# Performance work log

Measured on AMD Instinct MI355X. Metric: run time of the kernel, lower is better.

Reference implementation:

```python
import jax, jax.numpy as jnp
import numpy as np


def setup_inputs() -> dict:
    key = jax.random.key(0)
    k1, k2, k3, k4, k5 = jax.random.split(key, 5)
    B, C, D = 16384, 1000, 2048
    x = jax.random.normal(k1, (B, D), dtype=jnp.float32)
    W = jax.random.normal(k2, (C, D), dtype=jnp.float32) * 0.02  # fc weight
    b = jax.random.normal(k3, (C,), dtype=jnp.float32) * 0.01
    selector_weights = jax.random.normal(k4, (5,), dtype=jnp.float32) * 0.01
    selector_thresholds = jax.random.normal(k5, (5,), dtype=jnp.float32) * 0.01
    ensemble_threshold = jnp.zeros((1,), dtype=jnp.float32)
    return {
        "x": x, "W": W, "b": b,
        "selector_weights": selector_weights,
        "selector_thresholds": selector_thresholds,
        "ensemble_threshold": ensemble_threshold,
    }


def _selector_scores(logits, W):
    # top-2 of raw logits (RLConfM): sorted descending -> top_k(2)
    top2, _ = jax.lax.top_k(logits, 2)
    conf_m = top2[:, 0] - top2[:, 1]
    # geometric margin (RLGeoM): logits normalized by row norms of fc weight
    w_norms = jnp.linalg.norm(W, axis=1)                      # [C]
    norm_logits = logits / (w_norms + 1e-8)[None, :]          # [B, C]
    ntop2, _ = jax.lax.top_k(norm_logits, 2)
    geo_m = ntop2[:, 0] - ntop2[:, 1]
    # softmax-based selectors share one softmax pass
    probs = jax.nn.softmax(logits, axis=1)                    # [B, C]
    sr_max = jnp.max(probs, axis=1)
    doctor = 1.0 - 1.0 / jnp.sum(probs * probs, axis=1)
    neg_entropy = jnp.sum(probs * jnp.log(probs + 1e-10), axis=1)  # = -entropy
    # order matches nn.ModuleList: [SRMax, SRDoctor, SREntropy, RLGeoM, RLConfM]
    return jnp.stack([sr_max, doctor, neg_entropy, geo_m, conf_m], axis=1)  # [B, 5]


def reference(x, W, b, selector_weights, selector_thresholds, ensemble_threshold):
    # base model runs under no_grad in the original
    logits = jax.lax.stop_gradient(jnp.dot(x, W.T) + b)       # [B, C]
    scores = _selector_scores(logits, jax.lax.stop_gradient(W))  # [B, 5]
    indicators = jnp.tanh(scores - selector_thresholds[None, :])  # [B, 5]
    ensemble = jnp.sum(selector_weights[None, :] * indicators, axis=1)  # [B]
    selection_score = jnp.tanh(ensemble - ensemble_threshold[0])
    return (logits, selection_score)
```

## Files before the change

### kernel.cpp

```cpp
#include <hip/hip_runtime.h>
#include <stdint.h>

#define B_ROWS 16384
#define C_COLS 1000
#define D_DIM  2048

typedef __bf16 bf16x8 __attribute__((ext_vector_type(8)));
typedef float  f32x4  __attribute__((ext_vector_type(4)));
typedef unsigned short u16;

__device__ __forceinline__ u16 f2bf(float f) {
  union { float f; uint32_t u; } v; v.f = f;
  return (u16)((v.u + 0x7FFFu + ((v.u >> 16) & 1u)) >> 16);
}

__global__ __launch_bounds__(256)
void prep(const float* __restrict__ W, const float* __restrict__ x,
          u16* __restrict__ Wb, u16* __restrict__ xb, float* __restrict__ norms) {
  const int r = blockIdx.x;
  const int t = threadIdx.x;
  const bool isW = (r < C_COLS);
  const float* src = isW ? (W + (size_t)r * D_DIM)
                         : (x + (size_t)(r - C_COLS) * D_DIM);
  u16* dst = isW ? (Wb + (size_t)r * D_DIM)
                 : (xb + (size_t)(r - C_COLS) * D_DIM);
  const int c = t * 8;
  float4 v0 = *reinterpret_cast<const float4*>(src + c);
  float4 v1 = *reinterpret_cast<const float4*>(src + c + 4);
  uint32_t p0 = (uint32_t)f2bf(v0.x) | ((uint32_t)f2bf(v0.y) << 16);
  uint32_t p1 = (uint32_t)f2bf(v0.z) | ((uint32_t)f2bf(v0.w) << 16);
  uint32_t p2 = (uint32_t)f2bf(v1.x) | ((uint32_t)f2bf(v1.y) << 16);
  uint32_t p3 = (uint32_t)f2bf(v1.z) | ((uint32_t)f2bf(v1.w) << 16);
  const int row_id = isW ? r : (r - C_COLS);
  const int m2 = (row_id & 7) << 3;
  uint4 val; val.x = p0; val.y = p1; val.z = p2; val.w = p3;
  *reinterpret_cast<uint4*>(dst + (c ^ m2)) = val;
  if (isW) {
    float ss = v0.x*v0.x + v0.y*v0.y + v0.z*v0.z + v0.w*v0.w
             + v1.x*v1.x + v1.y*v1.y + v1.z*v1.z + v1.w*v1.w;
    #pragma unroll
    for (int m = 32; m; m >>= 1) ss += __shfl_xor(ss, m);
    __shared__ float wss[4];
    if ((t & 63) == 0) wss[t >> 6] = ss;
    __syncthreads();
    if (t == 0) norms[r] = sqrtf(wss[0] + wss[1] + wss[2] + wss[3]);
  }
}

#define ABASE(B,H) (((B)*2+(H))*8192)
#define BBASE(B,H) (32768 + ((B)*2+(H))*8192)

#define STAGE_A(BUF,H,OFF) { _Pragma("unroll") for (int j_=0;j_<2;++j_){ \
    u16* d_ = lds + ABASE(BUF,H) + (j_*64 + w*8)*64; \
    __builtin_amdgcn_global_load_lds( \
      (const __attribute__((address_space(1))) void*)(sa[H][j_] + (OFF)), \
      (__attribute__((address_space(3))) void*)d_, 16, 0, 0); } }

#define STAGE_B(BUF,H,OFF) { _Pragma("unroll") for (int j_=0;j_<2;++j_){ \
    u16* d_ = lds + BBASE(BUF,H) + (j_*64 + w*8)*64; \
    __builtin_amdgcn_global_load_lds( \
      (const __attribute__((address_space(1))) void*)(sb[H][j_] + (OFF)), \
      (__attribute__((address_space(3))) void*)d_, 16, 0, 0); } }

#define READ_A(BUF,MH) { _Pragma("unroll") for (int ks_=0;ks_<2;++ks_) \
  _Pragma("unroll") for (int fr_=0;fr_<4;++fr_) \
    Acur[ks_][fr_] = *reinterpret_cast<const bf16x8*>( \
        pA[ks_] + ((BUF)*2+(MH))*16384 + fr_*2048); }

#define READ_B(BUF,NH,DST) { _Pragma("unroll") for (int ks_=0;ks_<2;++ks_) \
  _Pragma("unroll") for (int fc_=0;fc_<2;++fc_) \
    DST[ks_][fc_] = *reinterpret_cast<const bf16x8*>( \
        pB[ks_] + ((BUF)*2+(NH))*16384 + fc_*2048); }

#define MMA(MH,NH,BSRC) { \
  __builtin_amdgcn_s_setprio(1); \
  _Pragma("unroll") for (int ks_=0;ks_<2;++ks_) \
    _Pragma("unroll") for (int fr_=0;fr_<4;++fr_) \
      _Pragma("unroll") for (int fc_=0;fc_<2;++fc_) \
        acc[MH][fr_][NH][fc_] = __builtin_amdgcn_mfma_f32_16x16x32_bf16( \
            Acur[ks_][fr_], BSRC[ks_][fc_], acc[MH][fr_][NH][fc_], 0, 0, 0); \
  __builtin_amdgcn_s_setprio(0); }

#define BAR  __builtin_amdgcn_s_barrier()
#define LG0  asm volatile("s_waitcnt lgkmcnt(0)" ::: "memory")
#define LG8  asm volatile("s_waitcnt lgkmcnt(8)" ::: "memory")
#define SCHB __builtin_amdgcn_sched_barrier(0)
#define VM4  asm volatile("s_waitcnt vmcnt(4)" ::: "memory")
#define VM0  asm volatile("s_waitcnt vmcnt(0)" ::: "memory")

#define SMERGE(m_,s_,q_,u_,om_,os_,oq_,ou_) { \
    float M_ = fmaxf(m_, om_); \
    float a_ = __expf(m_ - M_), b_ = __expf(om_ - M_); \
    float ns_ = a_*s_ + b_*os_; \
    float nq_ = a_*a_*q_ + b_*b_*oq_; \
    float nu_ = a_*(u_ + (m_-M_)*s_) + b_*(ou_ + (om_-M_)*os_); \
    m_ = M_; s_ = ns_; q_ = nq_; u_ = nu_; }

#define T2MERGE(t1_,t2_,o1_,o2_) { \
    if (o1_ > t1_) { t2_ = fmaxf(t1_, o2_); t1_ = o1_; } else t2_ = fmaxf(t2_, o1_); }

template<int FUSE>
__global__ __launch_bounds__(512, 2)
void gemm8(const u16* __restrict__ xb, const u16* __restrict__ Wb,
           const float* __restrict__ bias, float* __restrict__ out,
           const float* __restrict__ norms, float* __restrict__ partials) {
  __shared__ u16 lds[65536];

  const int bid = blockIdx.x;
  const int swz = (bid & 7) * 32 + (bid >> 3);
  const int tm = swz >> 2, tn = swz & 3;
  const int m0 = tm * 256, n0 = tn * 256;

  const int t = threadIdx.x, w = t >> 6, l = t & 63;
  const int wr = w >> 2, wcn = w & 3;

  f32x4 acc[2][4][2][2];
  #pragma unroll
  for (int a = 0; a < 2; ++a)
    #pragma unroll
    for (int b2 = 0; b2 < 4; ++b2)
      #pragma unroll
      for (int c2 = 0; c2 < 2; ++c2)
        #pragma unroll
        for (int d2 = 0; d2 < 2; ++d2)
          acc[a][b2][c2][d2] = (f32x4){0.f, 0.f, 0.f, 0.f};

  bf16x8 Acur[2][4], B0c[2][2], B1c[2][2];

  const char* ldsc = (const char*)lds;
  const int la  = l & 15;
  const int hi3 = (l >> 4) << 3;
  const int m3  = (l & 7) << 3;
  const char* pA[2];
  const char* pB[2];
  pA[0] = ldsc + wr*8192 + la*128 + (((0  + hi3) ^ m3) << 1);
  pA[1] = ldsc + wr*8192 + la*128 + (((32 + hi3) ^ m3) << 1);
  pB[0] = ldsc + 65536 + (wcn*32 + la)*128 + (((0  + hi3) ^ m3) << 1);
  pB[1] = ldsc + 65536 + (wcn*32 + la)*128 + (((32 + hi3) ^ m3) << 1);

  const char* sa[2][2];
  const char* sb[2][2];
  #pragma unroll
  for (int H = 0; H < 2; ++H)
    #pragma unroll
    for (int j = 0; j < 2; ++j) {
      sa[H][j] = (const char*)xb +
        (((size_t)(m0 + H*128 + j*64 + w*8 + (l>>3))) * D_DIM + (l&7)*8) * 2;
      int gr = n0 + H*128 + j*64 + w*8 + (l>>3);
      if (gr >= C_COLS) gr = C_COLS - 1;
      sb[H][j] = (const char*)Wb + ((size_t)gr * D_DIM + (l&7)*8) * 2;
    }

  STAGE_A(0,0,0); STAGE_B(0,0,0); STAGE_A(0,1,0); STAGE_B(0,1,0);
  STAGE_A(1,0,128); STAGE_B(1,0,128);
  VM4;
  BAR;

  for (int it = 0; it < 15; ++it) {
    READ_A(0,0); READ_B(0,0,B0c); READ_B(0,1,B1c);
    STAGE_A(1,1,128); STAGE_B(1,1,128); LG8;
    BAR; LG0; SCHB; MMA(0,0,B0c); MMA(0,1,B1c); BAR;
    READ_A(0,1); STAGE_A(0,0,256); STAGE_B(0,0,256);
    BAR; LG0; SCHB; MMA(1,1,B1c); MMA(1,0,B0c); VM4; BAR;
    READ_A(1,0); READ_B(1,0,B0c); READ_B(1,1,B1c);
    STAGE_A(0,1,256); STAGE_B(0,1,256); LG8;
    BAR; LG0; SCHB; MMA(0,0,B0c); MMA(0,1,B1c); BAR;
    READ_A(1,1); STAGE_A(1,0,384); STAGE_B(1,0,384);
    BAR; LG0; SCHB; MMA(1,1,B1c); MMA(1,0,B0c); VM4; BAR;
    #pragma unroll
    for (int H = 0; H < 2; ++H)
      #pragma unroll
      for (int j = 0; j < 2; ++j) { sa[H][j] += 256; sb[H][j] += 256; }
  }
  READ_A(0,0); READ_B(0,0,B0c); READ_B(0,1,B1c);
  STAGE_A(1,1,128); STAGE_B(1,1,128); LG8;
  BAR; LG0; SCHB; MMA(0,0,B0c); MMA(0,1,B1c); BAR;
  READ_A(0,1);
  BAR; LG0; SCHB; MMA(1,1,B1c); MMA(1,0,B0c); VM0; BAR;
  READ_A(1,0); READ_B(1,0,B0c); READ_B(1,1,B1c); LG8;
  BAR; LG0; SCHB; MMA(0,0,B0c); MMA(0,1,B1c); BAR;
  READ_A(1,1);
  BAR; LG0; SCHB; MMA(1,1,B1c); MMA(1,0,B0c);

  float bv[2][2]; bool okc[2][2];
  #pragma unroll
  for (int nh = 0; nh < 2; ++nh)
    #pragma unroll
    for (int fc = 0; fc < 2; ++fc) {
      int col = n0 + nh*128 + wcn*32 + fc*16 + (l & 15);
      okc[nh][fc] = (col < C_COLS);
      bv[nh][fc]  = okc[nh][fc] ? bias[col] : 0.f;
    }

  #pragma unroll
  for (int mh = 0; mh < 2; ++mh)
    #pragma unroll
    for (int nh = 0; nh < 2; ++nh)
      #pragma unroll
      for (int fc = 0; fc < 2; ++fc)
        if (okc[nh][fc]) {
          int col = n0 + nh*128 + wcn*32 + fc*16 + (l & 15);
          #pragma unroll
          for (int fr = 0; fr < 4; ++fr) {
            int row0 = m0 + mh*128 + wr*64 + fr*16 + ((l >> 4) << 2);
            #pragma unroll
            for (int j = 0; j < 4; ++j)
              out[(size_t)(row0 + j) * C_COLS + col] = acc[mh][fr][nh][fc][j] + bv[nh][fc];
          }
        }

  if constexpr (FUSE) {
    float* sf = (float*)lds;
    const int rrow = t >> 2;
    const int q    = t & 3;
    BAR;
    #pragma unroll
    for (int mh = 0; mh < 2; ++mh) {
      #pragma unroll
      for (int fr = 0; fr < 4; ++fr)
        #pragma unroll
        for (int j = 0; j < 4; ++j) {
          int rl = wr*64 + fr*16 + ((l >> 4) << 2) + j;
          int sw = (rl & 7) << 2;
          #pragma unroll
          for (int nh = 0; nh < 2; ++nh)
            #pragma unroll
            for (int fc = 0; fc < 2; ++fc) {
              int c = nh*128 + wcn*32 + fc*16 + (l & 15);
              sf[rl*256 + (c ^ sw)] = acc[mh][fr][nh][fc][j] + bv[nh][fc];
            }
        }
      LG0; BAR;
      float m=-3.4e38f, t1=-3.4e38f, t2=-3.4e38f, n1=-3.4e38f, n2=-3.4e38f;
      #pragma unroll
      for (int i = 0; i < 16; ++i) {
        int U = q*16 + i;
        f32x4 v4 = *reinterpret_cast<const f32x4*>(
            &sf[rrow*256 + 4*(U ^ (rrow & 7))]);
        f32x4 w4 = *reinterpret_cast<const f32x4*>(&norms[n0 + 4*U]);
        #pragma unroll
        for (int e = 0; e < 4; ++e) {
          int col = n0 + 4*U + e;
          if (col < C_COLS) {
            float v = v4[e];
            m = fmaxf(m, v);
            if (v > t1) { t2 = t1; t1 = v; } else if (v > t2) t2 = v;
            float nv = v / (w4[e] + 1e-8f);
            if (nv > n1) { n2 = n1; n1 = nv; } else if (nv > n2) n2 = nv;
          }
        }
      }
      float s = 0.f, qq = 0.f, u = 0.f;
      #pragma unroll
      for (int i = 0; i < 16; ++i) {
        int U = q*16 + i;
        f32x4 v4 = *reinterpret_cast<const f32x4*>(
            &sf[rrow*256 + 4*(U ^ (rrow & 7))]);
        #pragma unroll
        for (int e = 0; e < 4; ++e) {
          int col = n0 + 4*U + e;
          if (col < C_COLS) {
            float d = v4[e] - m;
            float ee = __expf(d);
            s += ee; qq += ee*ee; u += d*ee;
          }
        }
      }
      LG0;
      #pragma unroll
      for (int msk = 1; msk < 4; msk <<= 1) {
        float o1 = __shfl_xor(t1, msk), o2 = __shfl_xor(t2, msk);
        T2MERGE(t1, t2, o1, o2);
        float p1 = __shfl_xor(n1, msk), p2 = __shfl_xor(n2, msk);
        T2MERGE(n1, n2, p1, p2);
        float om = __shfl_xor(m, msk), os = __shfl_xor(s, msk);
        float oq = __shfl_xor(qq, msk), ou = __shfl_xor(u, msk);
        SMERGE(m, s, qq, u, om, os, oq, ou);
      }
      if (q == 0) {
        float* pp = partials + ((size_t)(m0 + mh*128 + rrow) * 4 + tn) * 8;
        float4 lo; lo.x=t1; lo.y=t2; lo.z=n1; lo.w=n2;
        float4 hi; hi.x=m;  hi.y=s;  hi.z=qq; hi.w=u;
        *reinterpret_cast<float4*>(pp)     = lo;
        *reinterpret_cast<float4*>(pp + 4) = hi;
      }
      if (mh == 0) { BAR; }
    }
  }
}

__global__ __launch_bounds__(256)
void selector2(const float* __restrict__ partials,
               const float* __restrict__ selw, const float* __restrict__ selt,
               const float* __restrict__ ethr, float* __restrict__ out2) {
  const int row = blockIdx.x * 256 + threadIdx.x;
  const float* pp = partials + (size_t)row * 32;
  float P[4][8];
  #pragma unroll
  for (int wv = 0; wv < 4; ++wv) {
    float4 lo = *reinterpret_cast<const float4*>(pp + wv*8);
    float4 hi = *reinterpret_cast<const float4*>(pp + wv*8 + 4);
    P[wv][0]=lo.x; P[wv][1]=lo.y; P[wv][2]=lo.z; P[wv][3]=lo.w;
    P[wv][4]=hi.x; P[wv][5]=hi.y; P[wv][6]=hi.z; P[wv][7]=hi.w;
  }
  float t1=P[0][0], t2=P[0][1], n1=P[0][2], n2=P[0][3];
  float m=P[0][4], s=P[0][5], q=P[0][6], u=P[0][7];
  #pragma unroll
  for (int wv = 1; wv < 4; ++wv) {
    T2MERGE(t1, t2, P[wv][0], P[wv][1]);
    T2MERGE(n1, n2, P[wv][2], P[wv][3]);
    SMERGE(m, s, q, u, P[wv][4], P[wv][5], P[wv][6], P[wv][7]);
  }
  float sc0 = 1.f / s;
  float sc1 = 1.f - (s * s) / q;
  float sc2 = u / s - __logf(s);
  float sc3 = n1 - n2;
  float sc4 = t1 - t2;
  float ens = selw[0] * tanhf(sc0 - selt[0])
            + selw[1] * tanhf(sc1 - selt[1])
            + selw[2] * tanhf(sc2 - selt[2])
            + selw[3] * tanhf(sc3 - selt[3])
            + selw[4] * tanhf(sc4 - selt[4]);
  out2[row] = tanhf(ens - ethr[0]);
}

__global__ __launch_bounds__(256)
void selector(const float* __restrict__ logits, const float* __restrict__ norms,
              const float* __restrict__ selw, const float* __restrict__ selt,
              const float* __restrict__ ethr, float* __restrict__ out) {
  __shared__ float nrm[1024];
  const int t = threadIdx.x;
  #pragma unroll
  for (int i = 0; i < 4; ++i) {
    int idx = t + i * 256;
    nrm[idx] = (idx < C_COLS) ? norms[idx] : 1.0f;
  }
  __syncthreads();
  const int w = t >> 6, l = t & 63;
  const int row = blockIdx.x * 4 + w;
  const float* lp = logits + (size_t)row * C_COLS;
  float lg[16];
  float t1 = -3.4e38f, t2 = -3.4e38f, n1 = -3.4e38f, n2 = -3.4e38f;
  #pragma unroll
  for (int i = 0; i < 4; ++i) {
    float4 v4 = *reinterpret_cast<const float4*>(lp + l * 4 + i * 256);
    #pragma unroll
    for (int j = 0; j < 4; ++j) {
      int idx = l * 4 + i * 256 + j;
      float raw = (j == 0) ? v4.x : (j == 1) ? v4.y : (j == 2) ? v4.z : v4.w;
      bool ok = (idx < C_COLS);
      float v = ok ? raw : -3.4e38f;
      lg[i * 4 + j] = v;
      if (v > t1) { t2 = t1; t1 = v; } else if (v > t2) t2 = v;
      float nv = ok ? raw / (nrm[idx] + 1e-8f) : -3.4e38f;
      if (nv > n1) { n2 = n1; n1 = nv; } else if (nv > n2) n2 = nv;
    }
  }
  #pragma unroll
  for (int m = 1; m < 64; m <<= 1) {
    float o1 = __shfl_xor(t1, m), o2 = __shfl_xor(t2, m);
    T2MERGE(t1, t2, o1, o2);
    float p1 = __shfl_xor(n1, m), p2 = __shfl_xor(n2, m);
    T2MERGE(n1, n2, p1, p2);
  }
  const float mx = t1;
  float S = 0.f, sq = 0.f;
  float ex[16];
  #pragma unroll
  for (int i = 0; i < 16; ++i) {
    float e = (lg[i] > -1e38f) ? __expf(lg[i] - mx) : 0.f;
    ex[i] = e; S += e; sq += e * e;
  }
  #pragma unroll
  for (int m = 1; m < 64; m <<= 1) { S += __shfl_xor(S, m); sq += __shfl_xor(sq, m); }
  float ent = 0.f;
  #pragma unroll
  for (int i = 0; i < 16; ++i)
    if (lg[i] > -1e38f) { float p = ex[i] / S; ent += p * __logf(p + 1e-10f); }
  #pragma unroll
  for (int m = 1; m < 64; m <<= 1) ent += __shfl_xor(ent, m);
  if (l == 0) {
    float ens = selw[0] * tanhf(1.f / S - selt[0])
              + selw[1] * tanhf(1.f - (S * S) / sq - selt[1])
              + selw[2] * tanhf(ent - selt[2])
              + selw[3] * tanhf(n1 - n2 - selt[3])
              + selw[4] * tanhf(t1 - t2 - selt[4]);
    out[row] = tanhf(ens - ethr[0]);
  }
}

extern "C" void kernel_launch(void* const* d_in, const int* in_sizes, int n_in,
                              void* d_out, int out_size, void* d_ws, size_t ws_size,
                              hipStream_t stream) {
  const float* x    = (const float*)d_in[0];
  const float* W    = (const float*)d_in[1];
  const float* b    = (const float*)d_in[2];
  const float* selw = (const float*)d_in[3];
  const float* selt = (const float*)d_in[4];
  const float* ethr = (const float*)d_in[5];
  float* out = (float*)d_out;
  float* out2 = out + (size_t)B_ROWS * C_COLS;

  u16*   Wb    = (u16*)d_ws;
  float* norms = (float*)((char*)d_ws + 4096000);
  u16*   xb    = (u16*)((char*)d_ws + 4100096);
  float* parts = (float*)((char*)d_ws + 4100096 + 67108864);

  const size_t need_fuse = 4100096 + 67108864 + 2097152;
  const size_t need_r4   = 4100096 + 67108864;

  if (ws_size >= need_fuse) {
    prep<<<C_COLS + B_ROWS, 256, 0, stream>>>(W, x, Wb, xb, norms);
    gemm8<1><<<256, 512, 0, stream>>>(xb, Wb, b, out, norms, parts);
    selector2<<<B_ROWS / 256, 256, 0, stream>>>(parts, selw, selt, ethr, out2);
  } else if (ws_size >= need_r4) {
    prep<<<C_COLS + B_ROWS, 256, 0, stream>>>(W, x, Wb, xb, norms);
    gemm8<0><<<256, 512, 0, stream>>>(xb, Wb, b, out, norms, nullptr);
    selector<<<B_ROWS / 4, 256, 0, stream>>>(out, norms, selw, selt, ethr, out2);
  }
}
```

Measured before the change: 124.0 us.

## Split MFMA by k-step with partial LDS waits and coalesce fused logits stores

The main loop now issues LDS fragment reads per k-substep. It waits only for the first substep's reads (lgkmcnt 8 or 4) before starting its MFMAs, so the second substep's LDS reads overlap with matrix math, and priority is raised across the whole MMA block. In the fused epilogue, logits are no longer scattered straight from MFMA accumulators to global memory. They are written as float4 vectors from the swizzled LDS tile already built for the selector reduction. The column interleave is changed so the four threads of a row write adjacent chunks. This adds a dependency on the finer waitcnt accounting and on C being a multiple of 4.

```diff
diff --git a/kernel.cpp b/kernel.cpp
--- a/kernel.cpp
+++ b/kernel.cpp
@@ -62,31 +62,30 @@
       (const __attribute__((address_space(1))) void*)(sb[H][j_] + (OFF)), \
       (__attribute__((address_space(3))) void*)d_, 16, 0, 0); } }
 
-#define READ_A(BUF,MH) { _Pragma("unroll") for (int ks_=0;ks_<2;++ks_) \
+#define READ_A_KS(BUF,MH,KS) { _Pragma("unroll") for (int fr_=0;fr_<4;++fr_) \
+    Acur[KS][fr_] = *reinterpret_cast<const bf16x8*>( \
+        pA[KS] + ((BUF)*2+(MH))*16384 + fr_*2048); }
+
+#define READ_B_KS(BUF,NH,DST,KS) { _Pragma("unroll") for (int fc_=0;fc_<2;++fc_) \
+    DST[KS][fc_] = *reinterpret_cast<const bf16x8*>( \
+        pB[KS] + ((BUF)*2+(NH))*16384 + fc_*2048); }
+
+#define MMAK(MH,NH,BSRC,KS) { \
   _Pragma("unroll") for (int fr_=0;fr_<4;++fr_) \
-    Acur[ks_][fr_] = *reinterpret_cast<const bf16x8*>( \
-        pA[ks_] + ((BUF)*2+(MH))*16384 + fr_*2048); }
-
-#define READ_B(BUF,NH,DST) { _Pragma("unroll") for (int ks_=0;ks_<2;++ks_) \
-  _Pragma("unroll") for (int fc_=0;fc_<2;++fc_) \
-    DST[ks_][fc_] = *reinterpret_cast<const bf16x8*>( \
-        pB[ks_] + ((BUF)*2+(NH))*16384 + fc_*2048); }
-
-#define MMA(MH,NH,BSRC) { \
-  __builtin_amdgcn_s_setprio(1); \
-  _Pragma("unroll") for (int ks_=0;ks_<2;++ks_) \
-    _Pragma("unroll") for (int fr_=0;fr_<4;++fr_) \
-      _Pragma("unroll") for (int fc_=0;fc_<2;++fc_) \
-        acc[MH][fr_][NH][fc_] = __builtin_amdgcn_mfma_f32_16x16x32_bf16( \
-            Acur[ks_][fr_], BSRC[ks_][fc_], acc[MH][fr_][NH][fc_], 0, 0, 0); \
-  __builtin_amdgcn_s_setprio(0); }
-
-#define BAR  __builtin_amdgcn_s_barrier()
-#define LG0  asm volatile("s_waitcnt lgkmcnt(0)" ::: "memory")
-#define LG8  asm volatile("s_waitcnt lgkmcnt(8)" ::: "memory")
-#define SCHB __builtin_amdgcn_sched_barrier(0)
-#define VM4  asm volatile("s_waitcnt vmcnt(4)" ::: "memory")
-#define VM0  asm volatile("s_waitcnt vmcnt(0)" ::: "memory")
+    _Pragma("unroll") for (int fc_=0;fc_<2;++fc_) \
+      acc[MH][fr_][NH][fc_] = __builtin_amdgcn_mfma_f32_16x16x32_bf16( \
+          Acur[KS][fr_], BSRC[KS][fc_], acc[MH][fr_][NH][fc_], 0, 0, 0); }
+
+#define BAR   __builtin_amdgcn_s_barrier()
+#define LG0   asm volatile("s_waitcnt lgkmcnt(0)" ::: "memory")
+#define LGK0  asm volatile("s_waitcnt lgkmcnt(0)" ::: "memory")
+#define LGK4  asm volatile("s_waitcnt lgkmcnt(4)" ::: "memory")
+#define LGK8  asm volatile("s_waitcnt lgkmcnt(8)" ::: "memory")
+#define SCHB  __builtin_amdgcn_sched_barrier(0)
+#define VM4   asm volatile("s_waitcnt vmcnt(4)" ::: "memory")
+#define VM0   asm volatile("s_waitcnt vmcnt(0)" ::: "memory")
+#define SETP1 __builtin_amdgcn_s_setprio(1)
+#define SETP0 __builtin_amdgcn_s_setprio(0)
 
 #define SMERGE(m_,s_,q_,u_,om_,os_,oq_,ou_) { \
     float M_ = fmaxf(m_, om_); \
@@ -157,30 +156,67 @@
   BAR;
 
   for (int it = 0; it < 15; ++it) {
-    READ_A(0,0); READ_B(0,0,B0c); READ_B(0,1,B1c);
-    STAGE_A(1,1,128); STAGE_B(1,1,128); LG8;
-    BAR; LG0; SCHB; MMA(0,0,B0c); MMA(0,1,B1c); BAR;
-    READ_A(0,1); STAGE_A(0,0,256); STAGE_B(0,0,256);
-    BAR; LG0; SCHB; MMA(1,1,B1c); MMA(1,0,B0c); VM4; BAR;
-    READ_A(1,0); READ_B(1,0,B0c); READ_B(1,1,B1c);
-    STAGE_A(0,1,256); STAGE_B(0,1,256); LG8;
-    BAR; LG0; SCHB; MMA(0,0,B0c); MMA(0,1,B1c); BAR;
-    READ_A(1,1); STAGE_A(1,0,384); STAGE_B(1,0,384);
-    BAR; LG0; SCHB; MMA(1,1,B1c); MMA(1,0,B0c); VM4; BAR;
+    READ_A_KS(0,0,0); READ_B_KS(0,0,B0c,0); READ_B_KS(0,1,B1c,0);
+    READ_A_KS(0,0,1); READ_B_KS(0,0,B0c,1); READ_B_KS(0,1,B1c,1);
+    STAGE_A(1,1,128); STAGE_B(1,1,128);
+    BAR; LGK8; SETP1; SCHB;
+    MMAK(0,0,B0c,0); MMAK(0,1,B1c,0);
+    LGK0; SCHB;
+    MMAK(0,0,B0c,1); MMAK(0,1,B1c,1); SETP0;
+    BAR;
+    READ_A_KS(0,1,0); READ_A_KS(0,1,1);
+    STAGE_A(0,0,256); STAGE_B(0,0,256);
+    BAR; LGK4; SETP1; SCHB;
+    MMAK(1,1,B1c,0); MMAK(1,0,B0c,0);
+    LGK0; SCHB;
+    MMAK(1,1,B1c,1); MMAK(1,0,B0c,1); SETP0;
+    VM4; BAR;
+    READ_A_KS(1,0,0); READ_B_KS(1,0,B0c,0); READ_B_KS(1,1,B1c,0);
+    READ_A_KS(1,0,1); READ_B_KS(1,0,B0c,1); READ_B_KS(1,1,B1c,1);
+    STAGE_A(0,1,256); STAGE_B(0,1,256);
+    BAR; LGK8; SETP1; SCHB;
+    MMAK(0,0,B0c,0); MMAK(0,1,B1c,0);
+    LGK0; SCHB;
+    MMAK(0,0,B0c,1); MMAK(0,1,B1c,1); SETP0;
+    BAR;
+    READ_A_KS(1,1,0); READ_A_KS(1,1,1);
+    STAGE_A(1,0,384); STAGE_B(1,0,384);
+    BAR; LGK4; SETP1; SCHB;
+    MMAK(1,1,B1c,0); MMAK(1,0,B0c,0);
+    LGK0; SCHB;
+    MMAK(1,1,B1c,1); MMAK(1,0,B0c,1); SETP0;
+    VM4; BAR;
     #pragma unroll
     for (int H = 0; H < 2; ++H)
       #pragma unroll
       for (int j = 0; j < 2; ++j) { sa[H][j] += 256; sb[H][j] += 256; }
   }
-  READ_A(0,0); READ_B(0,0,B0c); READ_B(0,1,B1c);
-  STAGE_A(1,1,128); STAGE_B(1,1,128); LG8;
-  BAR; LG0; SCHB; MMA(0,0,B0c); MMA(0,1,B1c); BAR;
-  READ_A(0,1);
-  BAR; LG0; SCHB; MMA(1,1,B1c); MMA(1,0,B0c); VM0; BAR;
-  READ_A(1,0); READ_B(1,0,B0c); READ_B(1,1,B1c); LG8;
-  BAR; LG0; SCHB; MMA(0,0,B0c); MMA(0,1,B1c); BAR;
-  READ_A(1,1);
-  BAR; LG0; SCHB; MMA(1,1,B1c); MMA(1,0,B0c);
+  READ_A_KS(0,0,0); READ_B_KS(0,0,B0c,0); READ_B_KS(0,1,B1c,0);
+  READ_A_KS(0,0,1); READ_B_KS(0,0,B0c,1); READ_B_KS(0,1,B1c,1);
+  STAGE_A(1,1,128); STAGE_B(1,1,128);
+  BAR; LGK8; SETP1; SCHB;
+  MMAK(0,0,B0c,0); MMAK(0,1,B1c,0);
+  LGK0; SCHB;
+  MMAK(0,0,B0c,1); MMAK(0,1,B1c,1); SETP0;
+  BAR;
+  READ_A_KS(0,1,0); READ_A_KS(0,1,1);
+  BAR; LGK4; SETP1; SCHB;
+  MMAK(1,1,B1c,0); MMAK(1,0,B0c,0);
+  LGK0; SCHB;
+  MMAK(1,1,B1c,1); MMAK(1,0,B0c,1); SETP0;
+  VM0; BAR;
+  READ_A_KS(1,0,0); READ_B_KS(1,0,B0c,0); READ_B_KS(1,1,B1c,0);
+  READ_A_KS(1,0,1); READ_B_KS(1,0,B0c,1); READ_B_KS(1,1,B1c,1);
+  BAR; LGK8; SETP1; SCHB;
+  MMAK(0,0,B0c,0); MMAK(0,1,B1c,0);
+  LGK0; SCHB;
+  MMAK(0,0,B0c,1); MMAK(0,1,B1c,1); SETP0;
+  BAR;
+  READ_A_KS(1,1,0); READ_A_KS(1,1,1);
+  BAR; LGK4; SETP1; SCHB;
+  MMAK(1,1,B1c,0); MMAK(1,0,B0c,0);
+  LGK0; SCHB;
+  MMAK(1,1,B1c,1); MMAK(1,0,B0c,1); SETP0;
 
   float bv[2][2]; bool okc[2][2];
   #pragma unroll
@@ -192,22 +228,24 @@
       bv[nh][fc]  = okc[nh][fc] ? bias[col] : 0.f;
     }
 
-  #pragma unroll
-  for (int mh = 0; mh < 2; ++mh)
-    #pragma unroll
-    for (int nh = 0; nh < 2; ++nh)
-      #pragma unroll
-      for (int fc = 0; fc < 2; ++fc)
-        if (okc[nh][fc]) {
-          int col = n0 + nh*128 + wcn*32 + fc*16 + (l & 15);
-          #pragma unroll
-          for (int fr = 0; fr < 4; ++fr) {
-            int row0 = m0 + mh*128 + wr*64 + fr*16 + ((l >> 4) << 2);
+  if constexpr (!FUSE) {
+    #pragma unroll
+    for (int mh = 0; mh < 2; ++mh)
+      #pragma unroll
+      for (int nh = 0; nh < 2; ++nh)
+        #pragma unroll
+        for (int fc = 0; fc < 2; ++fc)
+          if (okc[nh][fc]) {
+            int col = n0 + nh*128 + wcn*32 + fc*16 + (l & 15);
             #pragma unroll
-            for (int j = 0; j < 4; ++j)
-              out[(size_t)(row0 + j) * C_COLS + col] = acc[mh][fr][nh][fc][j] + bv[nh][fc];
+            for (int fr = 0; fr < 4; ++fr) {
+              int row0 = m0 + mh*128 + wr*64 + fr*16 + ((l >> 4) << 2);
+              #pragma unroll
+              for (int j = 0; j < 4; ++j)
+                out[(size_t)(row0 + j) * C_COLS + col] = acc[mh][fr][nh][fc][j] + bv[nh][fc];
+            }
           }
-        }
+  }
 
   if constexpr (FUSE) {
     float* sf = (float*)lds;
@@ -234,10 +272,13 @@
       float m=-3.4e38f, t1=-3.4e38f, t2=-3.4e38f, n1=-3.4e38f, n2=-3.4e38f;
       #pragma unroll
       for (int i = 0; i < 16; ++i) {
-        int U = q*16 + i;
+        int U = i*4 + q;
         f32x4 v4 = *reinterpret_cast<const f32x4*>(
             &sf[rrow*256 + 4*(U ^ (rrow & 7))]);
         f32x4 w4 = *reinterpret_cast<const f32x4*>(&norms[n0 + 4*U]);
+        if (n0 + 4*U + 3 < C_COLS)
+          *reinterpret_cast<f32x4*>(
+              &out[(size_t)(m0 + mh*128 + rrow) * C_COLS + n0 + 4*U]) = v4;
         #pragma unroll
         for (int e = 0; e < 4; ++e) {
           int col = n0 + 4*U + e;
@@ -253,7 +294,7 @@
       float s = 0.f, qq = 0.f, u = 0.f;
       #pragma unroll
       for (int i = 0; i < 16; ++i) {
-        int U = q*16 + i;
+        int U = i*4 + q;
         f32x4 v4 = *reinterpret_cast<const f32x4*>(
             &sf[rrow*256 + 4*(U ^ (rrow & 7))]);
         #pragma unroll
```

Result: faster. 117.3 us (median of 4 runs) (-5.4%).

## Shrink GEMM tile to 128x128 with 1024 blocks and fused coalesced logit store

Applied to the files above, without the earlier changes.

The fused GEMM moves from 256x256 output tiles (256 blocks) to 128x128 tiles (1024 blocks). LDS drops to 64KB and launch bounds allow 4 blocks per CU. The pipeline becomes a simple two-buffer phase loop that waits for all loads (vmcnt 0) at each step, and the per-row selector partials grow from 4 to 8 column tiles. Fused logits are now written from LDS as coalesced float4 rows instead of strided per-lane stores. The aim is better occupancy and load balance across CUs and cheaper output stores, at the cost of less operand reuse per tile, more global traffic, and a less overlapped load schedule.

```diff
diff --git a/kernel.cpp b/kernel.cpp
--- a/kernel.cpp
+++ b/kernel.cpp
@@ -47,46 +47,51 @@
   }
 }
 
-#define ABASE(B,H) (((B)*2+(H))*8192)
-#define BBASE(B,H) (32768 + ((B)*2+(H))*8192)
-
-#define STAGE_A(BUF,H,OFF) { _Pragma("unroll") for (int j_=0;j_<2;++j_){ \
-    u16* d_ = lds + ABASE(BUF,H) + (j_*64 + w*8)*64; \
+#define STAGE_A(BUF,OFF) { _Pragma("unroll") for (int j_=0;j_<2;++j_){ \
+    u16* d_ = lds + (BUF)*8192 + (j_*64 + w*8)*64; \
     __builtin_amdgcn_global_load_lds( \
-      (const __attribute__((address_space(1))) void*)(sa[H][j_] + (OFF)), \
+      (const __attribute__((address_space(1))) void*)(sa[j_] + (OFF)), \
       (__attribute__((address_space(3))) void*)d_, 16, 0, 0); } }
 
-#define STAGE_B(BUF,H,OFF) { _Pragma("unroll") for (int j_=0;j_<2;++j_){ \
-    u16* d_ = lds + BBASE(BUF,H) + (j_*64 + w*8)*64; \
+#define STAGE_B(BUF,OFF) { _Pragma("unroll") for (int j_=0;j_<2;++j_){ \
+    u16* d_ = lds + 16384 + (BUF)*8192 + (j_*64 + w*8)*64; \
     __builtin_amdgcn_global_load_lds( \
-      (const __attribute__((address_space(1))) void*)(sb[H][j_] + (OFF)), \
+      (const __attribute__((address_space(1))) void*)(sb[j_] + (OFF)), \
       (__attribute__((address_space(3))) void*)d_, 16, 0, 0); } }
 
-#define READ_A(BUF,MH) { _Pragma("unroll") for (int ks_=0;ks_<2;++ks_) \
+#define READ_A_KS(BUF,KS) { _Pragma("unroll") for (int fr_=0;fr_<4;++fr_) \
+    Af[KS][fr_] = *reinterpret_cast<const bf16x8*>( \
+        pA[KS] + (BUF)*16384 + fr_*2048); }
+
+#define READ_B_KS(BUF,KS) { _Pragma("unroll") for (int fc_=0;fc_<2;++fc_) \
+    Bf[KS][fc_] = *reinterpret_cast<const bf16x8*>( \
+        pB[KS] + (BUF)*16384 + fc_*2048); }
+
+#define MMA_KS(KS) { \
   _Pragma("unroll") for (int fr_=0;fr_<4;++fr_) \
-    Acur[ks_][fr_] = *reinterpret_cast<const bf16x8*>( \
-        pA[ks_] + ((BUF)*2+(MH))*16384 + fr_*2048); }
-
-#define READ_B(BUF,NH,DST) { _Pragma("unroll") for (int ks_=0;ks_<2;++ks_) \
-  _Pragma("unroll") for (int fc_=0;fc_<2;++fc_) \
-    DST[ks_][fc_] = *reinterpret_cast<const bf16x8*>( \
-        pB[ks_] + ((BUF)*2+(NH))*16384 + fc_*2048); }
-
-#define MMA(MH,NH,BSRC) { \
-  __builtin_amdgcn_s_setprio(1); \
-  _Pragma("unroll") for (int ks_=0;ks_<2;++ks_) \
-    _Pragma("unroll") for (int fr_=0;fr_<4;++fr_) \
-      _Pragma("unroll") for (int fc_=0;fc_<2;++fc_) \
-        acc[MH][fr_][NH][fc_] = __builtin_amdgcn_mfma_f32_16x16x32_bf16( \
-            Acur[ks_][fr_], BSRC[ks_][fc_], acc[MH][fr_][NH][fc_], 0, 0, 0); \
-  __builtin_amdgcn_s_setprio(0); }
-
-#define BAR  __builtin_amdgcn_s_barrier()
-#define LG0  asm volatile("s_waitcnt lgkmcnt(0)" ::: "memory")
-#define LG8  asm volatile("s_waitcnt lgkmcnt(8)" ::: "memory")
-#define SCHB __builtin_amdgcn_sched_barrier(0)
-#define VM4  asm volatile("s_waitcnt vmcnt(4)" ::: "memory")
-#define VM0  asm volatile("s_waitcnt vmcnt(0)" ::: "memory")
+    _Pragma("unroll") for (int fc_=0;fc_<2;++fc_) \
+      acc[fr_][fc_] = __builtin_amdgcn_mfma_f32_16x16x32_bf16( \
+          Af[KS][fr_], Bf[KS][fc_], acc[fr_][fc_], 0, 0, 0); }
+
+#define BAR   __builtin_amdgcn_s_barrier()
+#define LG0   asm volatile("s_waitcnt lgkmcnt(0)" ::: "memory")
+#define LGK0  asm volatile("s_waitcnt lgkmcnt(0)" ::: "memory")
+#define LGK6  asm volatile("s_waitcnt lgkmcnt(6)" ::: "memory")
+#define SCHB  __builtin_amdgcn_sched_barrier(0)
+#define VM0   asm volatile("s_waitcnt vmcnt(0)" ::: "memory")
+#define SETP1 __builtin_amdgcn_s_setprio(1)
+#define SETP0 __builtin_amdgcn_s_setprio(0)
+#define NOPV  ((void)0)
+
+#define PHASE(BUF,STG,VMW) { \
+  READ_A_KS(BUF,0); READ_B_KS(BUF,0); \
+  READ_A_KS(BUF,1); READ_B_KS(BUF,1); \
+  STG; \
+  BAR; LGK6; SETP1; SCHB; \
+  MMA_KS(0); \
+  LGK0; SCHB; \
+  MMA_KS(1); SETP0; \
+  VMW; BAR; }
 
 #define SMERGE(m_,s_,q_,u_,om_,os_,oq_,ou_) { \
     float M_ = fmaxf(m_, om_); \
@@ -100,32 +105,28 @@
     if (o1_ > t1_) { t2_ = fmaxf(t1_, o2_); t1_ = o1_; } else t2_ = fmaxf(t2_, o1_); }
 
 template<int FUSE>
-__global__ __launch_bounds__(512, 2)
+__global__ __launch_bounds__(512, 4)
 void gemm8(const u16* __restrict__ xb, const u16* __restrict__ Wb,
            const float* __restrict__ bias, float* __restrict__ out,
            const float* __restrict__ norms, float* __restrict__ partials) {
-  __shared__ u16 lds[65536];
+  __shared__ u16 lds[32768];
 
   const int bid = blockIdx.x;
-  const int swz = (bid & 7) * 32 + (bid >> 3);
-  const int tm = swz >> 2, tn = swz & 3;
-  const int m0 = tm * 256, n0 = tn * 256;
+  const int swz = (bid & 7) * 128 + (bid >> 3);
+  const int tm = swz >> 3, tn = swz & 7;
+  const int m0 = tm * 128, n0 = tn * 128;
 
   const int t = threadIdx.x, w = t >> 6, l = t & 63;
   const int wr = w >> 2, wcn = w & 3;
 
-  f32x4 acc[2][4][2][2];
-  #pragma unroll
-  for (int a = 0; a < 2; ++a)
-    #pragma unroll
-    for (int b2 = 0; b2 < 4; ++b2)
-      #pragma unroll
-      for (int c2 = 0; c2 < 2; ++c2)
-        #pragma unroll
-        for (int d2 = 0; d2 < 2; ++d2)
-          acc[a][b2][c2][d2] = (f32x4){0.f, 0.f, 0.f, 0.f};
-
-  bf16x8 Acur[2][4], B0c[2][2], B1c[2][2];
+  f32x4 acc[4][2];
+  #pragma unroll
+  for (int a = 0; a < 4; ++a)
+    #pragma unroll
+    for (int b2 = 0; b2 < 2; ++b2)
+      acc[a][b2] = (f32x4){0.f, 0.f, 0.f, 0.f};
+
+  bf16x8 Af[2][4], Bf[2][2];
 
   const char* ldsc = (const char*)lds;
   const int la  = l & 15;
@@ -135,79 +136,55 @@
   const char* pB[2];
   pA[0] = ldsc + wr*8192 + la*128 + (((0  + hi3) ^ m3) << 1);
   pA[1] = ldsc + wr*8192 + la*128 + (((32 + hi3) ^ m3) << 1);
-  pB[0] = ldsc + 65536 + (wcn*32 + la)*128 + (((0  + hi3) ^ m3) << 1);
-  pB[1] = ldsc + 65536 + (wcn*32 + la)*128 + (((32 + hi3) ^ m3) << 1);
-
-  const char* sa[2][2];
-  const char* sb[2][2];
-  #pragma unroll
-  for (int H = 0; H < 2; ++H)
-    #pragma unroll
-    for (int j = 0; j < 2; ++j) {
-      sa[H][j] = (const char*)xb +
-        (((size_t)(m0 + H*128 + j*64 + w*8 + (l>>3))) * D_DIM + (l&7)*8) * 2;
-      int gr = n0 + H*128 + j*64 + w*8 + (l>>3);
-      if (gr >= C_COLS) gr = C_COLS - 1;
-      sb[H][j] = (const char*)Wb + ((size_t)gr * D_DIM + (l&7)*8) * 2;
-    }
-
-  STAGE_A(0,0,0); STAGE_B(0,0,0); STAGE_A(0,1,0); STAGE_B(0,1,0);
-  STAGE_A(1,0,128); STAGE_B(1,0,128);
-  VM4;
+  pB[0] = ldsc + 32768 + wcn*4096 + la*128 + (((0  + hi3) ^ m3) << 1);
+  pB[1] = ldsc + 32768 + wcn*4096 + la*128 + (((32 + hi3) ^ m3) << 1);
+
+  const char* sa[2];
+  const char* sb[2];
+  #pragma unroll
+  for (int j = 0; j < 2; ++j) {
+    sa[j] = (const char*)xb +
+      (((size_t)(m0 + j*64 + w*8 + (l>>3))) * D_DIM + (l&7)*8) * 2;
+    int gr = n0 + j*64 + w*8 + (l>>3);
+    if (gr >= C_COLS) gr = C_COLS - 1;
+    sb[j] = (const char*)Wb + ((size_t)gr * D_DIM + (l&7)*8) * 2;
+  }
+
+  STAGE_A(0,0); STAGE_B(0,0);
+  VM0;
   BAR;
 
   for (int it = 0; it < 15; ++it) {
-    READ_A(0,0); READ_B(0,0,B0c); READ_B(0,1,B1c);
-    STAGE_A(1,1,128); STAGE_B(1,1,128); LG8;
-    BAR; LG0; SCHB; MMA(0,0,B0c); MMA(0,1,B1c); BAR;
-    READ_A(0,1); STAGE_A(0,0,256); STAGE_B(0,0,256);
-    BAR; LG0; SCHB; MMA(1,1,B1c); MMA(1,0,B0c); VM4; BAR;
-    READ_A(1,0); READ_B(1,0,B0c); READ_B(1,1,B1c);
-    STAGE_A(0,1,256); STAGE_B(0,1,256); LG8;
-    BAR; LG0; SCHB; MMA(0,0,B0c); MMA(0,1,B1c); BAR;
-    READ_A(1,1); STAGE_A(1,0,384); STAGE_B(1,0,384);
-    BAR; LG0; SCHB; MMA(1,1,B1c); MMA(1,0,B0c); VM4; BAR;
-    #pragma unroll
-    for (int H = 0; H < 2; ++H)
-      #pragma unroll
-      for (int j = 0; j < 2; ++j) { sa[H][j] += 256; sb[H][j] += 256; }
-  }
-  READ_A(0,0); READ_B(0,0,B0c); READ_B(0,1,B1c);
-  STAGE_A(1,1,128); STAGE_B(1,1,128); LG8;
-  BAR; LG0; SCHB; MMA(0,0,B0c); MMA(0,1,B1c); BAR;
-  READ_A(0,1);
-  BAR; LG0; SCHB; MMA(1,1,B1c); MMA(1,0,B0c); VM0; BAR;
-  READ_A(1,0); READ_B(1,0,B0c); READ_B(1,1,B1c); LG8;
-  BAR; LG0; SCHB; MMA(0,0,B0c); MMA(0,1,B1c); BAR;
-  READ_A(1,1);
-  BAR; LG0; SCHB; MMA(1,1,B1c); MMA(1,0,B0c);
-
-  float bv[2][2]; bool okc[2][2];
-  #pragma unroll
-  for (int nh = 0; nh < 2; ++nh)
-    #pragma unroll
-    for (int fc = 0; fc < 2; ++fc) {
-      int col = n0 + nh*128 + wcn*32 + fc*16 + (l & 15);
-      okc[nh][fc] = (col < C_COLS);
-      bv[nh][fc]  = okc[nh][fc] ? bias[col] : 0.f;
-    }
-
-  #pragma unroll
-  for (int mh = 0; mh < 2; ++mh)
-    #pragma unroll
-    for (int nh = 0; nh < 2; ++nh)
-      #pragma unroll
-      for (int fc = 0; fc < 2; ++fc)
-        if (okc[nh][fc]) {
-          int col = n0 + nh*128 + wcn*32 + fc*16 + (l & 15);
+    PHASE(0, { STAGE_A(1,128); STAGE_B(1,128); }, VM0);
+    PHASE(1, { STAGE_A(0,256); STAGE_B(0,256); }, VM0);
+    #pragma unroll
+    for (int j = 0; j < 2; ++j) { sa[j] += 256; sb[j] += 256; }
+  }
+  PHASE(0, { STAGE_A(1,128); STAGE_B(1,128); }, VM0);
+  PHASE(1, NOPV, NOPV);
+
+  float bv[2]; bool okc[2];
+  #pragma unroll
+  for (int fc = 0; fc < 2; ++fc) {
+    int col = n0 + wcn*32 + fc*16 + (l & 15);
+    okc[fc] = (col < C_COLS);
+    bv[fc]  = okc[fc] ? bias[col] : 0.f;
+  }
+
+  if constexpr (!FUSE) {
+    #pragma unroll
+    for (int fc = 0; fc < 2; ++fc)
+      if (okc[fc]) {
+        int col = n0 + wcn*32 + fc*16 + (l & 15);
+        #pragma unroll
+        for (int fr = 0; fr < 4; ++fr) {
+          int row0 = m0 + wr*64 + fr*16 + ((l >> 4) << 2);
           #pragma unroll
-          for (int fr = 0; fr < 4; ++fr) {
-            int row0 = m0 + mh*128 + wr*64 + fr*16 + ((l >> 4) << 2);
-            #pragma unroll
-            for (int j = 0; j < 4; ++j)
-              out[(size_t)(row0 + j) * C_COLS + col] = acc[mh][fr][nh][fc][j] + bv[nh][fc];
-          }
+          for (int j = 0; j < 4; ++j)
+            out[(size_t)(row0 + j) * C_COLS + col] = acc[fr][fc][j] + bv[fc];
         }
+      }
+  }
 
   if constexpr (FUSE) {
     float* sf = (float*)lds;
@@ -215,76 +192,73 @@
     const int q    = t & 3;
     BAR;
     #pragma unroll
-    for (int mh = 0; mh < 2; ++mh) {
+    for (int fr = 0; fr < 4; ++fr)
       #pragma unroll
-      for (int fr = 0; fr < 4; ++fr)
+      for (int j = 0; j < 4; ++j) {
+        int rl = wr*64 + fr*16 + ((l >> 4) << 2) + j;
+        int sw = (rl & 7) << 2;
         #pragma unroll
-        for (int j = 0; j < 4; ++j) {
-          int rl = wr*64 + fr*16 + ((l >> 4) << 2) + j;
-          int sw = (rl & 7) << 2;
-          #pragma unroll
-          for (int nh = 0; nh < 2; ++nh)
-            #pragma unroll
-            for (int fc = 0; fc < 2; ++fc) {
-              int c = nh*128 + wcn*32 + fc*16 + (l & 15);
-              sf[rl*256 + (c ^ sw)] = acc[mh][fr][nh][fc][j] + bv[nh][fc];
-            }
-        }
-      LG0; BAR;
-      float m=-3.4e38f, t1=-3.4e38f, t2=-3.4e38f, n1=-3.4e38f, n2=-3.4e38f;
-      #pragma unroll
-      for (int i = 0; i < 16; ++i) {
-        int U = q*16 + i;
-        f32x4 v4 = *reinterpret_cast<const f32x4*>(
-            &sf[rrow*256 + 4*(U ^ (rrow & 7))]);
-        f32x4 w4 = *reinterpret_cast<const f32x4*>(&norms[n0 + 4*U]);
-        #pragma unroll
-        for (int e = 0; e < 4; ++e) {
-          int col = n0 + 4*U + e;
-          if (col < C_COLS) {
-            float v = v4[e];
-            m = fmaxf(m, v);
-            if (v > t1) { t2 = t1; t1 = v; } else if (v > t2) t2 = v;
-            float nv = v / (w4[e] + 1e-8f);
-            if (nv > n1) { n2 = n1; n1 = nv; } else if (nv > n2) n2 = nv;
-          }
+        for (int fc = 0; fc < 2; ++fc) {
+          int c = wcn*32 + fc*16 + (l & 15);
+          sf[rl*128 + (c ^ sw)] = acc[fr][fc][j] + bv[fc];
         }
       }
-      float s = 0.f, qq = 0.f, u = 0.f;
+    LG0; BAR;
+    float m=-3.4e38f, t1=-3.4e38f, t2=-3.4e38f, n1=-3.4e38f, n2=-3.4e38f;
+    #pragma unroll
+    for (int i = 0; i < 8; ++i) {
+      int U = i*4 + q;
+      f32x4 v4 = *reinterpret_cast<const f32x4*>(
+          &sf[rrow*128 + 4*(U ^ (rrow & 7))]);
+      f32x4 w4 = *reinterpret_cast<const f32x4*>(&norms[n0 + 4*U]);
+      if (n0 + 4*U + 3 < C_COLS)
+        *reinterpret_cast<f32x4*>(
+            &out[(size_t)(m0 + rrow) * C_COLS + n0 + 4*U]) = v4;
       #pragma unroll
-      for (int i = 0; i < 16; ++i) {
-        int U = q*16 + i;
-        f32x4 v4 = *reinterpret_cast<const f32x4*>(
-            &sf[rrow*256 + 4*(U ^ (rrow & 7))]);
-        #pragma unroll
-        for (int e = 0; e < 4; ++e) {
-          int col = n0 + 4*U + e;
-          if (col < C_COLS) {
-            float d = v4[e] - m;
-            float ee = __expf(d);
-            s += ee; qq += ee*ee; u += d*ee;
-          }
+      for (int e = 0; e < 4; ++e) {
+        int col = n0 + 4*U + e;
+        if (col < C_COLS) {
+          float v = v4[e];
+          m = fmaxf(m, v);
+          if (v > t1) { t2 = t1; t1 = v; } else if (v > t2) t2 = v;
+          float nv = v / (w4[e] + 1e-8f);
+          if (nv > n1) { n2 = n1; n1 = nv; } else if (nv > n2) n2 = nv;
         }
       }
-      LG0;
+    }
+    float s = 0.f, qq = 0.f, u = 0.f;
+    #pragma unroll
+    for (int i = 0; i < 8; ++i) {
+      int U = i*4 + q;
+      f32x4 v4 = *reinterpret_cast<const f32x4*>(
+          &sf[rrow*128 + 4*(U ^ (rrow & 7))]);
       #pragma unroll
-      for (int msk = 1; msk < 4; msk <<= 1) {
-        float o1 = __shfl_xor(t1, msk), o2 = __shfl_xor(t2, msk);
-        T2MERGE(t1, t2, o1, o2);
-        float p1 = __shfl_xor(n1, msk), p2 = __shfl_xor(n2, msk);
-        T2MERGE(n1, n2, p1, p2);
-        float om = __shfl_xor(m, msk), os = __shfl_xor(s, msk);
-        float oq = __shfl_xor(qq, msk), ou = __shfl_xor(u, msk);
-        SMERGE(m, s, qq, u, om, os, oq, ou);
+      for (int e = 0; e < 4; ++e) {
+        int col = n0 + 4*U + e;
+        if (col < C_COLS) {
+          float d = v4[e] - m;
+          float ee = __expf(d);
+          s += ee; qq += ee*ee; u += d*ee;
+        }
       }
-      if (q == 0) {
-        float* pp = partials + ((size_t)(m0 + mh*128 + rrow) * 4 + tn) * 8;
-        float4 lo; lo.x=t1; lo.y=t2; lo.z=n1; lo.w=n2;
-        float4 hi; hi.x=m;  hi.y=s;  hi.z=qq; hi.w=u;
-        *reinterpret_cast<float4*>(pp)     = lo;
-        *reinterpret_cast<float4*>(pp + 4) = hi;
-      }
-      if (mh == 0) { BAR; }
+    }
+    LG0;
+    #pragma unroll
+    for (int msk = 1; msk < 4; msk <<= 1) {
+      float o1 = __shfl_xor(t1, msk), o2 = __shfl_xor(t2, msk);
+      T2MERGE(t1, t2, o1, o2);
+      float p1 = __shfl_xor(n1, msk), p2 = __shfl_xor(n2, msk);
+      T2MERGE(n1, n2, p1, p2);
+      float om = __shfl_xor(m, msk), os = __shfl_xor(s, msk);
+      float oq = __shfl_xor(qq, msk), ou = __shfl_xor(u, msk);
+      SMERGE(m, s, qq, u, om, os, oq, ou);
+    }
+    if (q == 0) {
+      float* pp = partials + ((size_t)(m0 + rrow) * 8 + tn) * 8;
+      float4 lo; lo.x=t1; lo.y=t2; lo.z=n1; lo.w=n2;
+      float4 hi; hi.x=m;  hi.y=s;  hi.z=qq; hi.w=u;
+      *reinterpret_cast<float4*>(pp)     = lo;
+      *reinterpret_cast<float4*>(pp + 4) = hi;
     }
   }
 }
@@ -294,22 +268,18 @@
                const float* __restrict__ selw, const float* __restrict__ selt,
                const float* __restrict__ ethr, float* __restrict__ out2) {
   const int row = blockIdx.x * 256 + threadIdx.x;
-  const float* pp = partials + (size_t)row * 32;
-  float P[4][8];
-  #pragma unroll
-  for (int wv = 0; wv < 4; ++wv) {
-    float4 lo = *reinterpret_cast<const float4*>(pp + wv*8);
-    float4 hi = *reinterpret_cast<const float4*>(pp + wv*8 + 4);
-    P[wv][0]=lo.x; P[wv][1]=lo.y; P[wv][2]=lo.z; P[wv][3]=lo.w;
-    P[wv][4]=hi.x; P[wv][5]=hi.y; P[wv][6]=hi.z; P[wv][7]=hi.w;
-  }
-  float t1=P[0][0], t2=P[0][1], n1=P[0][2], n2=P[0][3];
-  float m=P[0][4], s=P[0][5], q=P[0][6], u=P[0][7];
-  #pragma unroll
-  for (int wv = 1; wv < 4; ++wv) {
-    T2MERGE(t1, t2, P[wv][0], P[wv][1]);
-    T2MERGE(n1, n2, P[wv][2], P[wv][3]);
-    SMERGE(m, s, q, u, P[wv][4], P[wv][5], P[wv][6], P[wv][7]);
+  const float* pp = partials + (size_t)row * 64;
+  float4 lo = *reinterpret_cast<const float4*>(pp);
+  float4 hi = *reinterpret_cast<const float4*>(pp + 4);
+  float t1=lo.x, t2=lo.y, n1=lo.z, n2=lo.w;
+  float m=hi.x, s=hi.y, q=hi.z, u=hi.w;
+  #pragma unroll
+  for (int wv = 1; wv < 8; ++wv) {
+    float4 lo2 = *reinterpret_cast<const float4*>(pp + wv*8);
+    float4 hi2 = *reinterpret_cast<const float4*>(pp + wv*8 + 4);
+    T2MERGE(t1, t2, lo2.x, lo2.y);
+    T2MERGE(n1, n2, lo2.z, lo2.w);
+    SMERGE(m, s, q, u, hi2.x, hi2.y, hi2.z, hi2.w);
   }
   float sc0 = 1.f / s;
   float sc1 = 1.f - (s * s) / q;
@@ -406,16 +376,16 @@
   u16*   xb    = (u16*)((char*)d_ws + 4100096);
   float* parts = (float*)((char*)d_ws + 4100096 + 67108864);
 
-  const size_t need_fuse = 4100096 + 67108864 + 2097152;
-  const size_t need_r4   = 4100096 + 67108864;
+  const size_t need_fuse = 4100096 + 67108864 + 4194304;
+  const size_t need_min  = 4100096 + 67108864;
 
   if (ws_size >= need_fuse) {
     prep<<<C_COLS + B_ROWS, 256, 0, stream>>>(W, x, Wb, xb, norms);
-    gemm8<1><<<256, 512, 0, stream>>>(xb, Wb, b, out, norms, parts);
+    gemm8<1><<<1024, 512, 0, stream>>>(xb, Wb, b, out, norms, parts);
     selector2<<<B_ROWS / 256, 256, 0, stream>>>(parts, selw, selt, ethr, out2);
-  } else if (ws_size >= need_r4) {
+  } else if (ws_size >= need_min) {
     prep<<<C_COLS + B_ROWS, 256, 0, stream>>>(W, x, Wb, xb, norms);
-    gemm8<0><<<256, 512, 0, stream>>>(xb, Wb, b, out, norms, nullptr);
+    gemm8<0><<<1024, 512, 0, stream>>>(xb, Wb, b, out, norms, nullptr);
     selector<<<B_ROWS / 4, 256, 0, stream>>>(out, norms, selw, selt, ethr, out2);
   }
 }
```

After: 125.5 us. No clear change (+1.2%).
